# Kernel optimization log

Measured on AMD Instinct MI355X. Metric: run time of the kernel, lower is better.

The kernel has to match this reference:

```python
import jax, jax.numpy as jnp
import numpy as np

S = 16        # neighbor samples per layer
NL = 2        # number of GNN layers


def setup_inputs() -> dict:
    key = jax.random.key(0)
    ks = jax.random.split(key, 12)
    N_NODES, D, E, NMP, DEG, N_EDGE, B, NC = 50000, 128, 32, 3, 32, 200000, 1024, 8
    sc = 0.05
    return {
        "ids": jax.random.randint(ks[0], (B,), 0, N_NODES, dtype=jnp.int32),
        "feats": jax.random.normal(ks[1], (N_NODES, D), jnp.float32),
        "edge_emb": jax.random.normal(ks[2], (NMP, N_EDGE, E), jnp.float32),
        "adj_nodes": jax.random.randint(ks[3], (NMP, N_NODES, DEG), 0, N_NODES, dtype=jnp.int32),
        "adj_edges": jax.random.randint(ks[4], (NMP, N_NODES, DEG), 0, N_EDGE, dtype=jnp.int32),
        "W_self": jax.random.normal(ks[5], (NMP, NL, D, D), jnp.float32) * sc,
        "W_neigh": jax.random.normal(ks[6], (NMP, NL, D + E, D), jnp.float32) * sc,
        "W_edge": jax.random.normal(ks[7], (NMP, NL, 2 * D + E, E), jnp.float32) * sc,
        "attn": jax.random.normal(ks[8], (D,), jnp.float32) * sc,
        "fc_w": jax.random.normal(ks[9], (D, NC), jnp.float32) * sc,
        "fc_b": jnp.zeros((NC,), jnp.float32),
    }


def reference(ids, feats, edge_emb, adj_nodes, adj_edges, W_self, W_neigh, W_edge, attn, fc_w, fc_b):
    NMP = adj_nodes.shape[0]
    outs = []
    for mp in range(NMP):
        # --- sample neighbor tree (deterministic: first S columns) ---
        cur = ids
        all_feats = [feats[cur]]
        all_edges = []
        for _ in range(NL):
            nb = adj_nodes[mp][cur][:, :S].reshape(-1)     # [N*S]
            eid = adj_edges[mp][cur][:, :S].reshape(-1)    # [N*S]
            all_edges.append(edge_emb[mp][eid])            # [N*S, E]
            cur = nb
            all_feats.append(feats[cur])
        # --- per-layer aggregation + edge update ---
        for l in range(NL):
            new_feats = []
            for k in range(len(all_feats) - 1):
                xs, xn, ee = all_feats[k], all_feats[k + 1], all_edges[k]
                N = xs.shape[0]
                # mean over sampled neighbors of [neigh_feat || edge_emb]
                nin = jnp.concatenate(
                    [xn.reshape(N, S, -1), ee.reshape(N, S, -1)], axis=-1
                ).mean(axis=1)                             # [N, D+E]
                new_feats.append(jax.nn.relu(xs @ W_self[mp, l] + nin @ W_neigh[mp, l]))
            all_feats = new_feats  # dropout is identity in eval mode
            new_edges = []
            for k in range(len(all_edges) - 1):
                xs, xn, ee = all_feats[k], all_feats[k + 1], all_edges[k]
                rep = jnp.repeat(xs, S, axis=0)            # [N*S, D]
                new_edges.append(jax.nn.relu(
                    jnp.concatenate([rep, xn, ee], axis=-1) @ W_edge[mp, l]))
            all_edges = new_edges
        outs.append(all_feats[0])                          # [B, D]
    stacked = jnp.stack(outs)                              # [NMP, B, D]
    # metapath attention fuse
    scores = jnp.tanh(jnp.einsum('mbd,d->mb', stacked, attn))
    beta = jax.nn.softmax(scores, axis=0)
    emb = jnp.einsum('mb,mbd->bd', beta, stacked)          # [B, D]
    # F.normalize(dim=1)
    emb = emb / jnp.maximum(jnp.linalg.norm(emb, axis=1, keepdims=True), 1e-12)
    return emb @ fc_w + fc_b
```

## Files before the change

kernel.cpp:

```cpp
#include <hip/hip_runtime.h>

#define NNODES  50000
#define D       128
#define E       32
#define NMP     3
#define DEG     32
#define NEDGE   200000
#define B       1024
#define NC      8
#define S       16

#define RPM      17408
#define NKT      9
#define WSTRIDE  36864
#define WESTRIDE 9216

#define CONV_TASKS (1600000 + 6 * WSTRIDE + 3 * WESTRIDE)
#define TOT_TASKS  (CONV_TASKS + 3 * RPM)

typedef float f4 __attribute__((ext_vector_type(4)));
typedef short bh8 __attribute__((ext_vector_type(8)));
typedef unsigned int uv4 __attribute__((ext_vector_type(4)));
typedef unsigned int uv2 __attribute__((ext_vector_type(2)));
typedef int iv4 __attribute__((ext_vector_type(4)));
typedef int iv2 __attribute__((ext_vector_type(2)));

static __device__ __forceinline__ unsigned short f2bf(float f) {
    unsigned int u = __float_as_uint(f);
    u = u + 0x7FFFu + ((u >> 16) & 1u);
    return (unsigned short)(u >> 16);
}
static __device__ __forceinline__ float bf2f(unsigned short h) {
    return __uint_as_float(((unsigned int)h) << 16);
}

__global__ __launch_bounds__(256) void convsamp_k(
    const float* __restrict__ feats, const float* __restrict__ Ws,
    const float* __restrict__ Wn, const float* __restrict__ We,
    const int* __restrict__ ids, const int* __restrict__ adjn,
    const int* __restrict__ adje,
    unsigned short* __restrict__ fb, unsigned short* __restrict__ WT0,
    unsigned short* __restrict__ WTe, int* __restrict__ gx, int* __restrict__ eid1)
{
    int i = blockIdx.x * 256 + threadIdx.x;
    if (i < 1600000) {
        float4 v = ((const float4*)feats)[i];
        unsigned int p0 = (unsigned int)f2bf(v.x) | ((unsigned int)f2bf(v.y) << 16);
        unsigned int p1 = (unsigned int)f2bf(v.z) | ((unsigned int)f2bf(v.w) << 16);
        ((uint2*)fb)[i] = make_uint2(p0, p1);
    } else if (i < 1600000 + 6 * WSTRIDE) {
        int i2 = i - 1600000;
        int ml = i2 / WSTRIDE, e = i2 % WSTRIDE;
        int j = e & 7, t1 = e >> 3;
        int n = t1 & 127, t2 = t1 >> 7;
        int q = t2 & 3, kt = t2 >> 2;
        int k = kt * 32 + q * 8 + j;
        float v = (k < 128) ? Ws[((size_t)ml * 128 + k) * 128 + n]
                            : Wn[((size_t)ml * 160 + (k - 128)) * 128 + n];
        WT0[(size_t)ml * WSTRIDE + e] = f2bf(v);
    } else if (i < CONV_TASKS) {
        int i3 = i - 1600000 - 6 * WSTRIDE;
        int mp = i3 / WESTRIDE, e = i3 % WESTRIDE;
        int j = e & 7, t1 = e >> 3;
        int n = t1 & 31, t2 = t1 >> 5;
        int q = t2 & 3, kt = t2 >> 2;
        int k = kt * 32 + q * 8 + j;
        float v = We[(((size_t)mp * 2) * 288 + k) * 32 + n];
        WTe[(size_t)mp * WESTRIDE + e] = f2bf(v);
    } else if (i < TOT_TASKS) {
        int i4 = i - CONV_TASKS;
        int mp = i4 / RPM, r = i4 % RPM;
        if (r < 16384) {
            int node = ids[r >> 4];
            gx[mp * RPM + r]     = adjn[((size_t)mp * NNODES + node) * DEG + (r & 15)];
            eid1[mp * 16384 + r] = adje[((size_t)mp * NNODES + node) * DEG + (r & 15)];
        } else {
            gx[mp * RPM + r] = ids[r - 16384];
        }
    }
}

__global__ __launch_bounds__(256, 3) void aggfeat_k(
    const unsigned short* __restrict__ fb, const float* __restrict__ edge_emb,
    const int* __restrict__ adjn, const int* __restrict__ adje,
    const int* __restrict__ gx, const int* __restrict__ eid1,
    const unsigned short* __restrict__ WT0,
    unsigned short* __restrict__ fout)
{
    __shared__ unsigned short Asm[16][136];
    __shared__ unsigned short Nsm[16][168];
    const int mp = blockIdx.y;
    const int w = threadIdx.x >> 6, l = threadIdx.x & 63;
    const int r0 = blockIdx.x * 16;
    const unsigned int* fb32 = (const unsigned int*)fb;
    const float* ee = edge_emb + (size_t)mp * NEDGE * E;
    const float inv = 1.0f / (float)S;
    const int g = l >> 4, c = l & 15;
    const int d8 = l & 7;

    iv4 srcv = *(const iv4*)(gx + mp * RPM + r0 + w * 4);

    iv4 nIdx[4]; iv2 eIdx[4]; unsigned int selfu[4];
#pragma unroll
    for (int rr = 0; rr < 4; ++rr) {
        const int src = srcv[rr];
        nIdx[rr]  = *(const iv4*)(adjn + ((size_t)mp * NNODES + src) * DEG + 4 * g);
        eIdx[rr]  = *(const iv2*)(adje + ((size_t)mp * NNODES + src) * DEG + 2 * (l >> 3));
        selfu[rr] = fb32[(size_t)src * 64 + l];
    }

    uv4 gN[4][4];
    f4  gE[4][2];
#pragma unroll
    for (int rr = 0; rr < 4; ++rr) {
#pragma unroll
        for (int p = 0; p < 4; ++p)
            gN[rr][p] = *(const uv4*)(fb32 + (size_t)nIdx[rr][p] * 64 + c * 4);
        gE[rr][0] = *(const f4*)(ee + (size_t)eIdx[rr][0] * E + d8 * 4);
        gE[rr][1] = *(const f4*)(ee + (size_t)eIdx[rr][1] * E + d8 * 4);
    }
    asm volatile("" ::: "memory");

#pragma unroll
    for (int rr = 0; rr < 4; ++rr) {
        const int lr = w * 4 + rr;
        float acc[8];
#pragma unroll
        for (int d = 0; d < 8; ++d) acc[d] = 0.f;
#pragma unroll
        for (int p = 0; p < 4; ++p)
#pragma unroll
            for (int qq = 0; qq < 4; ++qq) {
                unsigned int u = gN[rr][p][qq];
                acc[2 * qq]     += __uint_as_float(u << 16);
                acc[2 * qq + 1] += __uint_as_float(u & 0xffff0000u);
            }
#pragma unroll
        for (int d = 0; d < 8; ++d) {
            acc[d] += __shfl_xor(acc[d], 16);
            acc[d] += __shfl_xor(acc[d], 32);
        }
        float fe[4];
#pragma unroll
        for (int qq = 0; qq < 4; ++qq) {
            fe[qq] = gE[rr][0][qq] + gE[rr][1][qq];
            fe[qq] += __shfl_xor(fe[qq], 8);
            fe[qq] += __shfl_xor(fe[qq], 16);
            fe[qq] += __shfl_xor(fe[qq], 32);
        }

        ((unsigned int*)&Asm[lr][0])[l] = selfu[rr];
        if (g == 0) {
            uv4 o;
#pragma unroll
            for (int qq = 0; qq < 4; ++qq)
                o[qq] = (unsigned int)f2bf(acc[2 * qq] * inv)
                      | ((unsigned int)f2bf(acc[2 * qq + 1] * inv) << 16);
            *(uv4*)&Nsm[lr][c * 8] = o;
        }
        if (l < 8) {
            uv2 o;
            o[0] = (unsigned int)f2bf(fe[0] * inv) | ((unsigned int)f2bf(fe[1] * inv) << 16);
            o[1] = (unsigned int)f2bf(fe[2] * inv) | ((unsigned int)f2bf(fe[3] * inv) << 16);
            *(uv2*)&Nsm[lr][128 + d8 * 4] = o;
        }
    }
    __syncthreads();

    const int q = l >> 4, lm = l & 15;
    const unsigned short* wb = WT0 + (size_t)mp * 2 * WSTRIDE;

    f4 acc[2];
    acc[0] = (f4){0.f, 0.f, 0.f, 0.f};
    acc[1] = (f4){0.f, 0.f, 0.f, 0.f};

#pragma unroll
    for (int kt = 0; kt < NKT; ++kt) {
        const int k0 = kt * 32 + q * 8;
        bh8 a = (k0 < 128) ? *(const bh8*)&Asm[lm][k0]
                           : *(const bh8*)&Nsm[lm][k0 - 128];
        const unsigned short* wrow = wb + ((size_t)(kt * 4 + q) * 128 + lm) * 8;
#pragma unroll
        for (int ntl = 0; ntl < 2; ++ntl) {
            bh8 bf = *(const bh8*)(wrow + (w * 2 + ntl) * 16 * 8);
            acc[ntl] = __builtin_amdgcn_mfma_f32_16x16x32_bf16(a, bf, acc[ntl], 0, 0, 0);
        }
    }

#pragma unroll
    for (int ntl = 0; ntl < 2; ++ntl)
#pragma unroll
        for (int rr = 0; rr < 4; ++rr) {
            int row = r0 + q * 4 + rr;
            int col = (w * 2 + ntl) * 16 + lm;
            fout[((size_t)mp * RPM + row) * 128 + col] = f2bf(fmaxf(acc[ntl][rr], 0.f));
        }
}

__global__ __launch_bounds__(256) void edgeagg_k(
    const unsigned short* __restrict__ fout, const float* __restrict__ edge_emb,
    const int* __restrict__ eid1, const unsigned short* __restrict__ WTe,
    const unsigned short* __restrict__ WT0,
    float* __restrict__ femb)
{
    __shared__ unsigned short As2[4][304];
    const int mp = blockIdx.y;
    const int w = threadIdx.x >> 6, l = threadIdx.x & 63;
    const int q = l >> 4, lm = l & 15;
    const int m0 = blockIdx.x * 64 + w * 16;
    const unsigned short* we = WTe + (size_t)mp * WESTRIDE;
    const unsigned short* f1base = fout + (size_t)mp * RPM * 128;
    const unsigned short* f0base = fout + ((size_t)mp * RPM + 16384) * 128;
    const float* ee = edge_emb + (size_t)mp * NEDGE * E;
    const float inv = 1.0f / (float)S;

    const int row = m0 + lm;
    const unsigned short* a1p = f1base + (size_t)row * 128;
    const unsigned short* a0p = f0base + (size_t)(row >> 4) * 128;
    const int eidL = eid1[mp * 16384 + row];

    f4 acc[2];
    acc[0] = (f4){0.f, 0.f, 0.f, 0.f};
    acc[1] = (f4){0.f, 0.f, 0.f, 0.f};

#pragma unroll
    for (int kt = 0; kt < NKT; ++kt) {
        const int k0 = kt * 32 + q * 8;
        bh8 a;
        if (kt < 4) {
            a = *(const bh8*)(a0p + k0);
        } else if (kt < 8) {
            a = *(const bh8*)(a1p + (k0 - 128));
        } else {
            const float* ep = ee + (size_t)eidL * E + q * 8;
            float4 v0 = *(const float4*)ep;
            float4 v1 = *(const float4*)(ep + 4);
            bh8 tv;
            tv[0] = (short)f2bf(v0.x); tv[1] = (short)f2bf(v0.y);
            tv[2] = (short)f2bf(v0.z); tv[3] = (short)f2bf(v0.w);
            tv[4] = (short)f2bf(v1.x); tv[5] = (short)f2bf(v1.y);
            tv[6] = (short)f2bf(v1.z); tv[7] = (short)f2bf(v1.w);
            a = tv;
        }
        const unsigned short* wrow = we + ((size_t)(kt * 4 + q) * 32 + lm) * 8;
        bh8 b0 = *(const bh8*)(wrow);
        bh8 b1 = *(const bh8*)(wrow + 16 * 8);
        acc[0] = __builtin_amdgcn_mfma_f32_16x16x32_bf16(a, b0, acc[0], 0, 0, 0);
        acc[1] = __builtin_amdgcn_mfma_f32_16x16x32_bf16(a, b1, acc[1], 0, 0, 0);
    }

#pragma unroll
    for (int nt = 0; nt < 2; ++nt) {
        float ps = 0.f;
#pragma unroll
        for (int rr = 0; rr < 4; ++rr) ps += fmaxf(acc[nt][rr], 0.f);
        ps += __shfl_xor(ps, 16);
        ps += __shfl_xor(ps, 32);
        if (l < 16)
            As2[w][256 + nt * 16 + lm] = f2bf(ps * inv);
    }

    {
        const int seg = m0 >> 4;
        unsigned int f0u = ((const unsigned int*)a0p)[l];
        ((unsigned int*)&As2[w][0])[l] = f0u;

        const unsigned short* fr = f1base + (size_t)seg * 16 * 128;
        float s0 = 0.f, s1 = 0.f;
#pragma unroll
        for (int j = 0; j < S; ++j) {
            unsigned int u = ((const unsigned int*)(fr + j * 128))[l];
            s0 += bf2f((unsigned short)(u & 0xFFFF));
            s1 += bf2f((unsigned short)(u >> 16));
        }
        ((unsigned int*)&As2[w][0])[64 + l] =
            (unsigned int)f2bf(s0 * inv) | ((unsigned int)f2bf(s1 * inv) << 16);
    }
    __syncthreads();

    const unsigned short* wb1 = WT0 + ((size_t)mp * 2 + 1) * WSTRIDE;
    f4 acc2[2];
    acc2[0] = (f4){0.f, 0.f, 0.f, 0.f};
    acc2[1] = (f4){0.f, 0.f, 0.f, 0.f};

#pragma unroll
    for (int kt = 0; kt < NKT; ++kt) {
        const int k0 = kt * 32 + q * 8;
        bh8 a;
        if (lm < 4) a = *(const bh8*)&As2[lm][k0];
        else        a = (bh8){0, 0, 0, 0, 0, 0, 0, 0};
        const unsigned short* wrow = wb1 + ((size_t)(kt * 4 + q) * 128 + lm) * 8;
#pragma unroll
        for (int ntl = 0; ntl < 2; ++ntl) {
            bh8 bf = *(const bh8*)(wrow + (w * 2 + ntl) * 16 * 8);
            acc2[ntl] = __builtin_amdgcn_mfma_f32_16x16x32_bf16(a, bf, acc2[ntl], 0, 0, 0);
        }
    }
    if (q == 0) {
#pragma unroll
        for (int ntl = 0; ntl < 2; ++ntl)
#pragma unroll
            for (int rr = 0; rr < 4; ++rr) {
                int seg = blockIdx.x * 4 + rr;
                femb[((size_t)mp * B + seg) * 128 + (w * 2 + ntl) * 16 + lm] =
                    fmaxf(acc2[ntl][rr], 0.f);
            }
    }
}

__global__ __launch_bounds__(256) void fin_k(
    const float* __restrict__ femb, const float* __restrict__ attn,
    const float* __restrict__ fcw, const float* __restrict__ fcb,
    float* __restrict__ out)
{
    const int row = blockIdx.x * 32 + (threadIdx.x >> 3);
    const int j = threadIdx.x & 7;
    const int d0 = j * 16;

    float v[NMP][16];
#pragma unroll
    for (int mp = 0; mp < NMP; ++mp)
#pragma unroll
        for (int t = 0; t < 4; ++t)
            *(f4*)&v[mp][t * 4] =
                *(const f4*)&femb[((size_t)mp * B + row) * 128 + d0 + t * 4];

    float sc[NMP];
#pragma unroll
    for (int mp = 0; mp < NMP; ++mp) {
        float p = 0.f;
#pragma unroll
        for (int d = 0; d < 16; ++d) p += v[mp][d] * attn[d0 + d];
        p += __shfl_xor(p, 1); p += __shfl_xor(p, 2); p += __shfl_xor(p, 4);
        sc[mp] = tanhf(p);
    }
    float mx = fmaxf(sc[0], fmaxf(sc[1], sc[2]));
    float e0 = expf(sc[0] - mx), e1 = expf(sc[1] - mx), e2 = expf(sc[2] - mx);
    float isum = 1.f / (e0 + e1 + e2);
    float b0 = e0 * isum, b1 = e1 * isum, b2 = e2 * isum;

    float emb[16];
    float nn = 0.f;
#pragma unroll
    for (int d = 0; d < 16; ++d) {
        float vv = b0 * v[0][d] + b1 * v[1][d] + b2 * v[2][d];
        emb[d] = vv;
        nn += vv * vv;
    }
    nn += __shfl_xor(nn, 1); nn += __shfl_xor(nn, 2); nn += __shfl_xor(nn, 4);
    float innorm = 1.f / fmaxf(sqrtf(nn), 1e-12f);
#pragma unroll
    for (int d = 0; d < 16; ++d) emb[d] *= innorm;

#pragma unroll
    for (int cc = 0; cc < NC; ++cc) {
        float p = 0.f;
#pragma unroll
        for (int d = 0; d < 16; ++d) p += emb[d] * fcw[(d0 + d) * NC + cc];
        p += __shfl_xor(p, 1); p += __shfl_xor(p, 2); p += __shfl_xor(p, 4);
        if (j == cc) out[(size_t)row * NC + cc] = p + fcb[cc];
    }
}

extern "C" void kernel_launch(void* const* d_in, const int* in_sizes, int n_in,
                              void* d_out, int out_size, void* d_ws, size_t ws_size,
                              hipStream_t stream) {
    const int* ids        = (const int*)d_in[0];
    const float* feats    = (const float*)d_in[1];
    const float* edge_emb = (const float*)d_in[2];
    const int* adjn       = (const int*)d_in[3];
    const int* adje       = (const int*)d_in[4];
    const float* Ws       = (const float*)d_in[5];
    const float* Wn       = (const float*)d_in[6];
    const float* We       = (const float*)d_in[7];
    const float* attn     = (const float*)d_in[8];
    const float* fcw      = (const float*)d_in[9];
    const float* fcb      = (const float*)d_in[10];
    float* out = (float*)d_out;

    char* p = (char*)d_ws;
    unsigned short* WT0 = (unsigned short*)p; p += (size_t)6 * WSTRIDE * 2;
    unsigned short* WTe = (unsigned short*)p; p += (size_t)3 * WESTRIDE * 2;
    unsigned short* fb  = (unsigned short*)p; p += (size_t)NNODES * 128 * 2;
    int* gx   = (int*)p;                      p += (size_t)3 * RPM * 4;
    int* eid1 = (int*)p;                      p += (size_t)3 * 16384 * 4;
    unsigned short* fout = (unsigned short*)p; p += (size_t)3 * RPM * 128 * 2;
    float* femb = (float*)p;                   p += (size_t)3 * B * 128 * 4;

    convsamp_k<<<TOT_TASKS / 256, 256, 0, stream>>>(feats, Ws, Wn, We, ids, adjn, adje,
                                                    fb, WT0, WTe, gx, eid1);
    aggfeat_k<<<dim3(RPM / 16, 3), 256, 0, stream>>>(fb, edge_emb, adjn, adje, gx, eid1,
                                                     WT0, fout);
    edgeagg_k<<<dim3(256, 3), 256, 0, stream>>>(fout, edge_emb, eid1, WTe, WT0, femb);
    fin_k<<<32, 256, 0, stream>>>(femb, attn, fcw, fcb, out);
}
```

Baseline: 224.8 us.

## Fuse edge aggregation and final attention/classifier into one kernel

Merges edgeagg_k and fin_k into a single kernel. Each block now loops over the three metapaths instead of using a grid y-dimension, and keeps the per-metapath embeddings in shared memory. The attention fuse, normalization and FC then run in the same block, which removes one launch and the femb round trip through global memory. In exchange the grid shrinks from 768 to 256 blocks with serial per-metapath work per block, which lowers parallelism on a large GPU.

```diff
diff --git a/kernel.cpp b/kernel.cpp
--- a/kernel.cpp
+++ b/kernel.cpp
@@ -197,168 +197,160 @@
         }
 }
 
-__global__ __launch_bounds__(256) void edgeagg_k(
+__global__ __launch_bounds__(256) void edgeaggfin_k(
     const unsigned short* __restrict__ fout, const float* __restrict__ edge_emb,
     const int* __restrict__ eid1, const unsigned short* __restrict__ WTe,
     const unsigned short* __restrict__ WT0,
-    float* __restrict__ femb)
+    const float* __restrict__ attn, const float* __restrict__ fcw,
+    const float* __restrict__ fcb, float* __restrict__ out)
 {
     __shared__ unsigned short As2[4][304];
-    const int mp = blockIdx.y;
+    __shared__ float fembs[NMP][4][128];
     const int w = threadIdx.x >> 6, l = threadIdx.x & 63;
     const int q = l >> 4, lm = l & 15;
-    const int m0 = blockIdx.x * 64 + w * 16;
-    const unsigned short* we = WTe + (size_t)mp * WESTRIDE;
-    const unsigned short* f1base = fout + (size_t)mp * RPM * 128;
-    const unsigned short* f0base = fout + ((size_t)mp * RPM + 16384) * 128;
-    const float* ee = edge_emb + (size_t)mp * NEDGE * E;
     const float inv = 1.0f / (float)S;
 
-    const int row = m0 + lm;
-    const unsigned short* a1p = f1base + (size_t)row * 128;
-    const unsigned short* a0p = f0base + (size_t)(row >> 4) * 128;
-    const int eidL = eid1[mp * 16384 + row];
-
-    f4 acc[2];
-    acc[0] = (f4){0.f, 0.f, 0.f, 0.f};
-    acc[1] = (f4){0.f, 0.f, 0.f, 0.f};
-
-#pragma unroll
-    for (int kt = 0; kt < NKT; ++kt) {
-        const int k0 = kt * 32 + q * 8;
-        bh8 a;
-        if (kt < 4) {
-            a = *(const bh8*)(a0p + k0);
-        } else if (kt < 8) {
-            a = *(const bh8*)(a1p + (k0 - 128));
-        } else {
-            const float* ep = ee + (size_t)eidL * E + q * 8;
-            float4 v0 = *(const float4*)ep;
-            float4 v1 = *(const float4*)(ep + 4);
-            bh8 tv;
-            tv[0] = (short)f2bf(v0.x); tv[1] = (short)f2bf(v0.y);
-            tv[2] = (short)f2bf(v0.z); tv[3] = (short)f2bf(v0.w);
-            tv[4] = (short)f2bf(v1.x); tv[5] = (short)f2bf(v1.y);
-            tv[6] = (short)f2bf(v1.z); tv[7] = (short)f2bf(v1.w);
-            a = tv;
-        }
-        const unsigned short* wrow = we + ((size_t)(kt * 4 + q) * 32 + lm) * 8;
-        bh8 b0 = *(const bh8*)(wrow);
-        bh8 b1 = *(const bh8*)(wrow + 16 * 8);
-        acc[0] = __builtin_amdgcn_mfma_f32_16x16x32_bf16(a, b0, acc[0], 0, 0, 0);
-        acc[1] = __builtin_amdgcn_mfma_f32_16x16x32_bf16(a, b1, acc[1], 0, 0, 0);
-    }
-
-#pragma unroll
-    for (int nt = 0; nt < 2; ++nt) {
-        float ps = 0.f;
-#pragma unroll
-        for (int rr = 0; rr < 4; ++rr) ps += fmaxf(acc[nt][rr], 0.f);
-        ps += __shfl_xor(ps, 16);
-        ps += __shfl_xor(ps, 32);
-        if (l < 16)
-            As2[w][256 + nt * 16 + lm] = f2bf(ps * inv);
-    }
-
-    {
-        const int seg = m0 >> 4;
-        unsigned int f0u = ((const unsigned int*)a0p)[l];
-        ((unsigned int*)&As2[w][0])[l] = f0u;
-
-        const unsigned short* fr = f1base + (size_t)seg * 16 * 128;
-        float s0 = 0.f, s1 = 0.f;
-#pragma unroll
-        for (int j = 0; j < S; ++j) {
-            unsigned int u = ((const unsigned int*)(fr + j * 128))[l];
-            s0 += bf2f((unsigned short)(u & 0xFFFF));
-            s1 += bf2f((unsigned short)(u >> 16));
-        }
-        ((unsigned int*)&As2[w][0])[64 + l] =
-            (unsigned int)f2bf(s0 * inv) | ((unsigned int)f2bf(s1 * inv) << 16);
-    }
-    __syncthreads();
-
-    const unsigned short* wb1 = WT0 + ((size_t)mp * 2 + 1) * WSTRIDE;
-    f4 acc2[2];
-    acc2[0] = (f4){0.f, 0.f, 0.f, 0.f};
-    acc2[1] = (f4){0.f, 0.f, 0.f, 0.f};
-
-#pragma unroll
-    for (int kt = 0; kt < NKT; ++kt) {
-        const int k0 = kt * 32 + q * 8;
-        bh8 a;
-        if (lm < 4) a = *(const bh8*)&As2[lm][k0];
-        else        a = (bh8){0, 0, 0, 0, 0, 0, 0, 0};
-        const unsigned short* wrow = wb1 + ((size_t)(kt * 4 + q) * 128 + lm) * 8;
-#pragma unroll
-        for (int ntl = 0; ntl < 2; ++ntl) {
-            bh8 bf = *(const bh8*)(wrow + (w * 2 + ntl) * 16 * 8);
-            acc2[ntl] = __builtin_amdgcn_mfma_f32_16x16x32_bf16(a, bf, acc2[ntl], 0, 0, 0);
-        }
-    }
-    if (q == 0) {
-#pragma unroll
-        for (int ntl = 0; ntl < 2; ++ntl)
-#pragma unroll
-            for (int rr = 0; rr < 4; ++rr) {
-                int seg = blockIdx.x * 4 + rr;
-                femb[((size_t)mp * B + seg) * 128 + (w * 2 + ntl) * 16 + lm] =
-                    fmaxf(acc2[ntl][rr], 0.f);
+    for (int mp = 0; mp < NMP; ++mp) {
+        const int m0 = (blockIdx.x * 4 + w) * 16;
+        const unsigned short* we = WTe + (size_t)mp * WESTRIDE;
+        const unsigned short* f1base = fout + (size_t)mp * RPM * 128;
+        const unsigned short* f0base = fout + ((size_t)mp * RPM + 16384) * 128;
+        const float* ee = edge_emb + (size_t)mp * NEDGE * E;
+
+        const int row = m0 + lm;
+        const unsigned short* a1p = f1base + (size_t)row * 128;
+        const unsigned short* a0p = f0base + (size_t)(row >> 4) * 128;
+        const int eidL = eid1[mp * 16384 + row];
+
+        f4 acc[2];
+        acc[0] = (f4){0.f, 0.f, 0.f, 0.f};
+        acc[1] = (f4){0.f, 0.f, 0.f, 0.f};
+
+#pragma unroll
+        for (int kt = 0; kt < NKT; ++kt) {
+            const int k0 = kt * 32 + q * 8;
+            bh8 a;
+            if (kt < 4) {
+                a = *(const bh8*)(a0p + k0);
+            } else if (kt < 8) {
+                a = *(const bh8*)(a1p + (k0 - 128));
+            } else {
+                const float* ep = ee + (size_t)eidL * E + q * 8;
+                float4 v0 = *(const float4*)ep;
+                float4 v1 = *(const float4*)(ep + 4);
+                bh8 tv;
+                tv[0] = (short)f2bf(v0.x); tv[1] = (short)f2bf(v0.y);
+                tv[2] = (short)f2bf(v0.z); tv[3] = (short)f2bf(v0.w);
+                tv[4] = (short)f2bf(v1.x); tv[5] = (short)f2bf(v1.y);
+                tv[6] = (short)f2bf(v1.z); tv[7] = (short)f2bf(v1.w);
+                a = tv;
             }
-    }
-}
-
-__global__ __launch_bounds__(256) void fin_k(
-    const float* __restrict__ femb, const float* __restrict__ attn,
-    const float* __restrict__ fcw, const float* __restrict__ fcb,
-    float* __restrict__ out)
-{
-    const int row = blockIdx.x * 32 + (threadIdx.x >> 3);
-    const int j = threadIdx.x & 7;
-    const int d0 = j * 16;
-
-    float v[NMP][16];
-#pragma unroll
-    for (int mp = 0; mp < NMP; ++mp)
-#pragma unroll
-        for (int t = 0; t < 4; ++t)
-            *(f4*)&v[mp][t * 4] =
-                *(const f4*)&femb[((size_t)mp * B + row) * 128 + d0 + t * 4];
-
-    float sc[NMP];
-#pragma unroll
-    for (int mp = 0; mp < NMP; ++mp) {
-        float p = 0.f;
-#pragma unroll
-        for (int d = 0; d < 16; ++d) p += v[mp][d] * attn[d0 + d];
-        p += __shfl_xor(p, 1); p += __shfl_xor(p, 2); p += __shfl_xor(p, 4);
-        sc[mp] = tanhf(p);
-    }
-    float mx = fmaxf(sc[0], fmaxf(sc[1], sc[2]));
-    float e0 = expf(sc[0] - mx), e1 = expf(sc[1] - mx), e2 = expf(sc[2] - mx);
-    float isum = 1.f / (e0 + e1 + e2);
-    float b0 = e0 * isum, b1 = e1 * isum, b2 = e2 * isum;
-
-    float emb[16];
-    float nn = 0.f;
-#pragma unroll
-    for (int d = 0; d < 16; ++d) {
-        float vv = b0 * v[0][d] + b1 * v[1][d] + b2 * v[2][d];
-        emb[d] = vv;
-        nn += vv * vv;
-    }
-    nn += __shfl_xor(nn, 1); nn += __shfl_xor(nn, 2); nn += __shfl_xor(nn, 4);
-    float innorm = 1.f / fmaxf(sqrtf(nn), 1e-12f);
-#pragma unroll
-    for (int d = 0; d < 16; ++d) emb[d] *= innorm;
-
-#pragma unroll
-    for (int cc = 0; cc < NC; ++cc) {
-        float p = 0.f;
-#pragma unroll
-        for (int d = 0; d < 16; ++d) p += emb[d] * fcw[(d0 + d) * NC + cc];
-        p += __shfl_xor(p, 1); p += __shfl_xor(p, 2); p += __shfl_xor(p, 4);
-        if (j == cc) out[(size_t)row * NC + cc] = p + fcb[cc];
+            const unsigned short* wrow = we + ((size_t)(kt * 4 + q) * 32 + lm) * 8;
+            bh8 b0 = *(const bh8*)(wrow);
+            bh8 b1 = *(const bh8*)(wrow + 16 * 8);
+            acc[0] = __builtin_amdgcn_mfma_f32_16x16x32_bf16(a, b0, acc[0], 0, 0, 0);
+            acc[1] = __builtin_amdgcn_mfma_f32_16x16x32_bf16(a, b1, acc[1], 0, 0, 0);
+        }
+
+#pragma unroll
+        for (int nt = 0; nt < 2; ++nt) {
+            float ps = 0.f;
+#pragma unroll
+            for (int rr = 0; rr < 4; ++rr) ps += fmaxf(acc[nt][rr], 0.f);
+            ps += __shfl_xor(ps, 16);
+            ps += __shfl_xor(ps, 32);
+            if (l < 16)
+                As2[w][256 + nt * 16 + lm] = f2bf(ps * inv);
+        }
+
+        {
+            const int seg = m0 >> 4;
+            unsigned int f0u = ((const unsigned int*)a0p)[l];
+            ((unsigned int*)&As2[w][0])[l] = f0u;
+
+            const unsigned short* fr = f1base + (size_t)seg * 16 * 128;
+            float s0 = 0.f, s1 = 0.f;
+#pragma unroll
+            for (int j = 0; j < S; ++j) {
+                unsigned int u = ((const unsigned int*)(fr + j * 128))[l];
+                s0 += bf2f((unsigned short)(u & 0xFFFF));
+                s1 += bf2f((unsigned short)(u >> 16));
+            }
+            ((unsigned int*)&As2[w][0])[64 + l] =
+                (unsigned int)f2bf(s0 * inv) | ((unsigned int)f2bf(s1 * inv) << 16);
+        }
+        __syncthreads();
+
+        const unsigned short* wb1 = WT0 + ((size_t)mp * 2 + 1) * WSTRIDE;
+        f4 acc2[2];
+        acc2[0] = (f4){0.f, 0.f, 0.f, 0.f};
+        acc2[1] = (f4){0.f, 0.f, 0.f, 0.f};
+
+#pragma unroll
+        for (int kt = 0; kt < NKT; ++kt) {
+            const int k0 = kt * 32 + q * 8;
+            bh8 a;
+            if (lm < 4) a = *(const bh8*)&As2[lm][k0];
+            else        a = (bh8){0, 0, 0, 0, 0, 0, 0, 0};
+            const unsigned short* wrow = wb1 + ((size_t)(kt * 4 + q) * 128 + lm) * 8;
+#pragma unroll
+            for (int ntl = 0; ntl < 2; ++ntl) {
+                bh8 bf = *(const bh8*)(wrow + (w * 2 + ntl) * 16 * 8);
+                acc2[ntl] = __builtin_amdgcn_mfma_f32_16x16x32_bf16(a, bf, acc2[ntl], 0, 0, 0);
+            }
+        }
+        if (q == 0) {
+#pragma unroll
+            for (int ntl = 0; ntl < 2; ++ntl)
+#pragma unroll
+                for (int rr = 0; rr < 4; ++rr)
+                    fembs[mp][rr][(w * 2 + ntl) * 16 + lm] = fmaxf(acc2[ntl][rr], 0.f);
+        }
+        __syncthreads();
+    }
+
+    if (threadIdx.x < 32) {
+        const int row = threadIdx.x >> 3;
+        const int j = threadIdx.x & 7;
+        const int d0 = j * 16;
+
+        float sc[NMP];
+#pragma unroll
+        for (int mp = 0; mp < NMP; ++mp) {
+            float p = 0.f;
+#pragma unroll
+            for (int d = 0; d < 16; ++d) p += fembs[mp][row][d0 + d] * attn[d0 + d];
+            p += __shfl_xor(p, 1); p += __shfl_xor(p, 2); p += __shfl_xor(p, 4);
+            sc[mp] = tanhf(p);
+        }
+        float mx = fmaxf(sc[0], fmaxf(sc[1], sc[2]));
+        float e0 = expf(sc[0] - mx), e1 = expf(sc[1] - mx), e2 = expf(sc[2] - mx);
+        float isum = 1.f / (e0 + e1 + e2);
+        float b0 = e0 * isum, b1 = e1 * isum, b2 = e2 * isum;
+
+        float emb[16];
+        float nn = 0.f;
+#pragma unroll
+        for (int d = 0; d < 16; ++d) {
+            float vv = b0 * fembs[0][row][d0 + d] + b1 * fembs[1][row][d0 + d]
+                     + b2 * fembs[2][row][d0 + d];
+            emb[d] = vv;
+            nn += vv * vv;
+        }
+        nn += __shfl_xor(nn, 1); nn += __shfl_xor(nn, 2); nn += __shfl_xor(nn, 4);
+        float innorm = 1.f / fmaxf(sqrtf(nn), 1e-12f);
+#pragma unroll
+        for (int d = 0; d < 16; ++d) emb[d] *= innorm;
+
+        const int grow = blockIdx.x * 4 + row;
+#pragma unroll
+        for (int cc = 0; cc < NC; ++cc) {
+            float p = 0.f;
+#pragma unroll
+            for (int d = 0; d < 16; ++d) p += emb[d] * fcw[(d0 + d) * NC + cc];
+            p += __shfl_xor(p, 1); p += __shfl_xor(p, 2); p += __shfl_xor(p, 4);
+            if (j == cc) out[(size_t)grow * NC + cc] = p + fcb[cc];
+        }
     }
 }
 
@@ -385,12 +377,11 @@
     int* gx   = (int*)p;                      p += (size_t)3 * RPM * 4;
     int* eid1 = (int*)p;                      p += (size_t)3 * 16384 * 4;
     unsigned short* fout = (unsigned short*)p; p += (size_t)3 * RPM * 128 * 2;
-    float* femb = (float*)p;                   p += (size_t)3 * B * 128 * 4;
 
     convsamp_k<<<TOT_TASKS / 256, 256, 0, stream>>>(feats, Ws, Wn, We, ids, adjn, adje,
                                                     fb, WT0, WTe, gx, eid1);
     aggfeat_k<<<dim3(RPM / 16, 3), 256, 0, stream>>>(fb, edge_emb, adjn, adje, gx, eid1,
                                                      WT0, fout);
-    edgeagg_k<<<dim3(256, 3), 256, 0, stream>>>(fout, edge_emb, eid1, WTe, WT0, femb);
-    fin_k<<<32, 256, 0, stream>>>(femb, attn, fcw, fcb, out);
-}
+    edgeaggfin_k<<<256, 256, 0, stream>>>(fout, edge_emb, eid1, WTe, WT0,
+                                          attn, fcw, fcb, out);
+}
```

Result: no change. 225.9 us (+0.5%).
